# Optimization experiments

Measured on AMD Instinct MI355X. Metric: run time of the kernel, lower is better.

The kernel has to match this reference:

```python
import jax, jax.numpy as jnp
import numpy as np

HIDDEN = 1024
VOCAB = 50257
MAX_LEN = 512


def setup_inputs() -> dict:
    key = jax.random.key(0)
    ks = jax.random.split(key, 16)
    s = 0.02
    return {
        # forward args
        "input_token": jax.random.randint(ks[0], (1,), 0, VOCAB),
        "hidden": jax.random.normal(ks[1], (1, 1, HIDDEN), jnp.float32),
        "encoder_outputs": jax.random.normal(ks[2], (MAX_LEN, HIDDEN), jnp.float32),
        # learned parameters
        "emb": jax.random.normal(ks[3], (VOCAB, HIDDEN), jnp.float32) * s,
        "attn_W": jax.random.normal(ks[4], (MAX_LEN, 2 * HIDDEN), jnp.float32) * s,
        "attn_b": jnp.zeros((MAX_LEN,), jnp.float32),
        "comb_W": jax.random.normal(ks[5], (HIDDEN, 2 * HIDDEN), jnp.float32) * s,
        "comb_b": jnp.zeros((HIDDEN,), jnp.float32),
        "W_ih": jax.random.normal(ks[6], (3 * HIDDEN, HIDDEN), jnp.float32) * s,
        "W_hh": jax.random.normal(ks[7], (3 * HIDDEN, HIDDEN), jnp.float32) * s,
        "b_ih": jnp.zeros((3 * HIDDEN,), jnp.float32),
        "b_hh": jnp.zeros((3 * HIDDEN,), jnp.float32),
        "out_W": jax.random.normal(ks[8], (VOCAB, HIDDEN), jnp.float32) * s,
        "out_b": jnp.zeros((VOCAB,), jnp.float32),
    }


def reference(input_token, hidden, encoder_outputs, emb, attn_W, attn_b,
              comb_W, comb_b, W_ih, W_hh, b_ih, b_hh, out_W, out_b):
    H = hidden.shape[-1]
    # embedding lookup: [1, H]; dropout=0.0 -> identity
    embed = emb[input_token]
    h0 = hidden[0]  # [1, H]
    # Bahdanau-style attention over encoder outputs
    cat = jnp.concatenate([embed, h0], axis=1)                 # [1, 2H]
    attn_weights = jax.nn.softmax(cat @ attn_W.T + attn_b, axis=1)  # [1, L]
    attn_applied = attn_weights @ encoder_outputs              # [1, H]
    # combine + relu
    x = jnp.concatenate([embed, attn_applied], axis=1) @ comb_W.T + comb_b
    x = jax.nn.relu(x)                                         # [1, H]
    # single GRU step (PyTorch gate ordering: r, z, n)
    gi = x @ W_ih.T + b_ih    # [1, 3H]
    gh = h0 @ W_hh.T + b_hh   # [1, 3H]
    i_r, i_z, i_n = gi[:, :H], gi[:, H:2 * H], gi[:, 2 * H:]
    h_r, h_z, h_n = gh[:, :H], gh[:, H:2 * H], gh[:, 2 * H:]
    r = jax.nn.sigmoid(i_r + h_r)
    z = jax.nn.sigmoid(i_z + h_z)
    n = jnp.tanh(i_n + r * h_n)
    h_new = (1.0 - z) * n + z * h0                             # [1, H]
    # output projection + log-softmax
    logp = jax.nn.log_softmax(h_new @ out_W.T + out_b, axis=1)  # [1, V]
    return logp, h_new[None], attn_weights
```

## Files before the change

kernel.cpp:

```cpp
#include <hip/hip_runtime.h>
#include <math.h>

#define H 1024
#define V 50257
#define L 512

#define S_SCORES   0
#define S_ATTN     1024
#define S_X        2048
#define S_GI       3072
#define S_GH       6144
#define S_HNEW     9216
#define S_LOGITS   10240
#define S_PART     60512
#define S_PARTIALS 76928
#define S_RED      102064

#define NB_LOGITS  12565

__device__ __forceinline__ float dot4(float4 a, float4 b) {
  return a.x*b.x + a.y*b.y + a.z*b.z + a.w*b.w;
}

__device__ __forceinline__ float wred_sum(float v) {
  #pragma unroll
  for (int o = 32; o > 0; o >>= 1) v += __shfl_down(v, o, 64);
  return v;
}

__device__ __forceinline__ float wred_max(float v) {
  #pragma unroll
  for (int o = 32; o > 0; o >>= 1) v = fmaxf(v, __shfl_down(v, o, 64));
  return v;
}

__global__ void k_scores(const int* __restrict__ tok, const float* __restrict__ h0,
                         const float* __restrict__ emb, const float* __restrict__ attn_W,
                         const float* __restrict__ attn_b, float* __restrict__ ws) {
  __shared__ float red[4];
  int t = threadIdx.x, lane = t & 63, wid = t >> 6;
  int j = blockIdx.x;
  const float4* wr = (const float4*)(attn_W + (size_t)j * (2 * H));
  const float4* e4 = (const float4*)(emb + (size_t)tok[0] * H);
  const float4* h4 = (const float4*)h0;
  float v = dot4(wr[t], e4[t]) + dot4(wr[256 + t], h4[t]);
  v = wred_sum(v);
  if (lane == 0) red[wid] = v;
  __syncthreads();
  if (t == 0) ws[S_SCORES + j] = red[0] + red[1] + red[2] + red[3] + attn_b[j];
}

__global__ void k_softmax_attn(const float* __restrict__ enc, float* __restrict__ ws,
                               float* __restrict__ out) {
  __shared__ float w[512];
  __shared__ float red[4];
  int t = threadIdx.x, lane = t & 63, wid = t >> 6;
  float s0 = ws[S_SCORES + t], s1 = ws[S_SCORES + 256 + t];
  float m = wred_max(fmaxf(s0, s1));
  if (lane == 0) red[wid] = m;
  __syncthreads();
  m = fmaxf(fmaxf(red[0], red[1]), fmaxf(red[2], red[3]));
  __syncthreads();
  float e0 = expf(s0 - m), e1 = expf(s1 - m);
  float ls = wred_sum(e0 + e1);
  if (lane == 0) red[wid] = ls;
  __syncthreads();
  float inv = 1.0f / (red[0] + red[1] + red[2] + red[3]);
  w[t] = e0 * inv;
  w[256 + t] = e1 * inv;
  __syncthreads();
  if (blockIdx.x == 0) {
    out[V + H + t] = w[t];
    out[V + H + 256 + t] = w[256 + t];
  }
  int cc = blockIdx.x & 3, rc = blockIdx.x >> 2;
  int col = cc * 256 + t;
  int j0 = rc * 32;
  float acc = 0.f;
  #pragma unroll 8
  for (int j = 0; j < 32; ++j) acc += w[j0 + j] * enc[(size_t)(j0 + j) * H + col];
  ws[S_PART + (size_t)rc * H + col] = acc;
}

__global__ void k_attn_reduce(float* __restrict__ ws) {
  int col = blockIdx.x * 256 + threadIdx.x;
  float acc = 0.f;
  #pragma unroll
  for (int p = 0; p < 16; ++p) acc += ws[S_PART + (size_t)p * H + col];
  ws[S_ATTN + col] = acc;
}

__global__ void k_comb(const int* __restrict__ tok, const float* __restrict__ emb,
                       const float* __restrict__ comb_W, const float* __restrict__ comb_b,
                       float* __restrict__ ws) {
  int t = threadIdx.x, lane = t & 63, wid = t >> 6;
  int row = blockIdx.x * 4 + wid;
  const float4* wr = (const float4*)(comb_W + (size_t)row * (2 * H));
  const float4* e4 = (const float4*)(emb + (size_t)tok[0] * H);
  const float4* a4 = (const float4*)(ws + S_ATTN);
  float v = 0.f;
  #pragma unroll
  for (int k = 0; k < 4; ++k) v += dot4(wr[lane + 64 * k], e4[lane + 64 * k]);
  #pragma unroll
  for (int k = 0; k < 4; ++k) v += dot4(wr[256 + lane + 64 * k], a4[lane + 64 * k]);
  v = wred_sum(v);
  if (lane == 0) ws[S_X + row] = fmaxf(v + comb_b[row], 0.f);
}

__global__ void k_gates(const float* __restrict__ h0, const float* __restrict__ W_ih,
                        const float* __restrict__ W_hh, const float* __restrict__ b_ih,
                        const float* __restrict__ b_hh, float* __restrict__ ws) {
  int t = threadIdx.x, lane = t & 63, wid = t >> 6;
  int g = blockIdx.x * 4 + wid;
  const float* Wp;
  const float4* vec;
  float bias;
  int dst;
  if (g < 3 * H) {
    Wp = W_ih + (size_t)g * H;
    vec = (const float4*)(ws + S_X);
    bias = b_ih[g];
    dst = S_GI + g;
  } else {
    int r = g - 3 * H;
    Wp = W_hh + (size_t)r * H;
    vec = (const float4*)h0;
    bias = b_hh[r];
    dst = S_GH + r;
  }
  const float4* wr = (const float4*)Wp;
  float v = 0.f;
  #pragma unroll
  for (int k = 0; k < 4; ++k) v += dot4(wr[lane + 64 * k], vec[lane + 64 * k]);
  v = wred_sum(v);
  if (lane == 0) ws[dst] = v + bias;
}

__global__ void k_gru(const float* __restrict__ h0, float* __restrict__ ws,
                      float* __restrict__ out) {
  int i = blockIdx.x * 256 + threadIdx.x;
  float ir = ws[S_GI + i], iz = ws[S_GI + H + i], in_ = ws[S_GI + 2 * H + i];
  float hr = ws[S_GH + i], hz = ws[S_GH + H + i], hn = ws[S_GH + 2 * H + i];
  float r = 1.f / (1.f + expf(-(ir + hr)));
  float z = 1.f / (1.f + expf(-(iz + hz)));
  float n = tanhf(in_ + r * hn);
  float h = (1.f - z) * n + z * h0[i];
  ws[S_HNEW + i] = h;
  out[V + i] = h;
}

__global__ void k_logits(const float* __restrict__ out_W, const float* __restrict__ out_b,
                         float* __restrict__ ws) {
  __shared__ float hl[H];
  __shared__ float wl[4];
  int t = threadIdx.x, lane = t & 63, wid = t >> 6;
  ((float4*)hl)[t] = ((const float4*)(ws + S_HNEW))[t];
  __syncthreads();
  int row = blockIdx.x * 4 + wid;
  float logit = -INFINITY;
  if (row < V) {
    const float4* wr = (const float4*)(out_W + (size_t)row * H);
    const float4* h4 = (const float4*)hl;
    float v = 0.f;
    #pragma unroll
    for (int k = 0; k < 4; ++k) v += dot4(wr[lane + 64 * k], h4[lane + 64 * k]);
    v = wred_sum(v);
    if (lane == 0) {
      logit = v + out_b[row];
      ws[S_LOGITS + row] = logit;
    }
  }
  if (lane == 0) wl[wid] = logit;
  __syncthreads();
  if (t == 0) {
    float m = fmaxf(fmaxf(wl[0], wl[1]), fmaxf(wl[2], wl[3]));
    float s = 0.f;
    #pragma unroll
    for (int i = 0; i < 4; ++i)
      if (wl[i] != -INFINITY) s += expf(wl[i] - m);
    ws[S_PARTIALS + 2 * blockIdx.x] = m;
    ws[S_PARTIALS + 2 * blockIdx.x + 1] = s;
  }
}

__device__ __forceinline__ void lse_merge(float& m, float& s, float mb, float sb) {
  if (mb == -INFINITY) return;
  if (m == -INFINITY) { m = mb; s = sb; return; }
  if (mb > m) { float tm = m; m = mb; mb = tm; float ts = s; s = sb; sb = ts; }
  s += sb * expf(mb - m);
}

__global__ void k_combine(float* __restrict__ ws) {
  __shared__ float lm[4], lsv[4];
  int t = threadIdx.x, lane = t & 63, wid = t >> 6;
  float m = -INFINITY, s = 0.f;
  for (int i = t; i < NB_LOGITS; i += 256)
    lse_merge(m, s, ws[S_PARTIALS + 2 * i], ws[S_PARTIALS + 2 * i + 1]);
  #pragma unroll
  for (int o = 32; o > 0; o >>= 1) {
    float mb = __shfl_down(m, o, 64);
    float sb = __shfl_down(s, o, 64);
    lse_merge(m, s, mb, sb);
  }
  if (lane == 0) { lm[wid] = m; lsv[wid] = s; }
  __syncthreads();
  if (t == 0) {
    float M = lm[0], S = lsv[0];
    #pragma unroll
    for (int i = 1; i < 4; ++i) lse_merge(M, S, lm[i], lsv[i]);
    ws[S_RED] = M + logf(S);
  }
}

__global__ void k_logp(const float* __restrict__ ws, float* __restrict__ out) {
  int i = blockIdx.x * 256 + threadIdx.x;
  if (i < V) out[i] = ws[S_LOGITS + i] - ws[S_RED];
}

extern "C" void kernel_launch(void* const* d_in, const int* in_sizes, int n_in,
                              void* d_out, int out_size, void* d_ws, size_t ws_size,
                              hipStream_t stream) {
  const int* tok = (const int*)d_in[0];
  const float* hidden = (const float*)d_in[1];
  const float* enc = (const float*)d_in[2];
  const float* emb = (const float*)d_in[3];
  const float* attn_W = (const float*)d_in[4];
  const float* attn_b = (const float*)d_in[5];
  const float* comb_W = (const float*)d_in[6];
  const float* comb_b = (const float*)d_in[7];
  const float* W_ih = (const float*)d_in[8];
  const float* W_hh = (const float*)d_in[9];
  const float* b_ih = (const float*)d_in[10];
  const float* b_hh = (const float*)d_in[11];
  const float* out_W = (const float*)d_in[12];
  const float* out_b = (const float*)d_in[13];
  float* out = (float*)d_out;
  float* ws = (float*)d_ws;

  hipLaunchKernelGGL(k_scores, dim3(512), dim3(256), 0, stream, tok, hidden, emb, attn_W, attn_b, ws);
  hipLaunchKernelGGL(k_softmax_attn, dim3(64), dim3(256), 0, stream, enc, ws, out);
  hipLaunchKernelGGL(k_attn_reduce, dim3(4), dim3(256), 0, stream, ws);
  hipLaunchKernelGGL(k_comb, dim3(256), dim3(256), 0, stream, tok, emb, comb_W, comb_b, ws);
  hipLaunchKernelGGL(k_gates, dim3(1536), dim3(256), 0, stream, hidden, W_ih, W_hh, b_ih, b_hh, ws);
  hipLaunchKernelGGL(k_gru, dim3(4), dim3(256), 0, stream, hidden, ws, out);
  hipLaunchKernelGGL(k_logits, dim3(NB_LOGITS), dim3(256), 0, stream, out_W, out_b, ws);
  hipLaunchKernelGGL(k_combine, dim3(1), dim3(256), 0, stream, ws);
  hipLaunchKernelGGL(k_logp, dim3((V + 255) / 256), dim3(256), 0, stream, ws, out);
}
```

Before: 439.6 us.

## Fuse attention reduce into combine, write logits in place, widen logits blocks

Removes the separate attention-partials reduction kernel by summing the 16 partials inside the combine kernel. Logits are now written straight into the output buffer, and the final kernel subtracts the log-sum-exp in place, which drops a workspace round trip. The logits kernel handles 16 rows per block (4 per wave) to cut block count and partial count, and the scores kernel uses one wave per row. In exchange, the combine kernel repeats the partial reduction in every block, and each wave issues fewer parallel loads, which may lower memory-level parallelism.

```diff
diff --git a/kernel.cpp b/kernel.cpp
--- a/kernel.cpp
+++ b/kernel.cpp
@@ -6,17 +6,15 @@
 #define L 512
 
 #define S_SCORES   0
-#define S_ATTN     1024
 #define S_X        2048
 #define S_GI       3072
 #define S_GH       6144
 #define S_HNEW     9216
-#define S_LOGITS   10240
-#define S_PART     60512
-#define S_PARTIALS 76928
-#define S_RED      102064
-
-#define NB_LOGITS  12565
+#define S_PART     10240
+#define S_PARTIALS 26624
+#define S_RED      33000
+
+#define NB_LOGITS  3142
 
 __device__ __forceinline__ float dot4(float4 a, float4 b) {
   return a.x*b.x + a.y*b.y + a.z*b.z + a.w*b.w;
@@ -37,17 +35,19 @@
 __global__ void k_scores(const int* __restrict__ tok, const float* __restrict__ h0,
                          const float* __restrict__ emb, const float* __restrict__ attn_W,
                          const float* __restrict__ attn_b, float* __restrict__ ws) {
-  __shared__ float red[4];
-  int t = threadIdx.x, lane = t & 63, wid = t >> 6;
-  int j = blockIdx.x;
+  int t = threadIdx.x, lane = t & 63, wid = t >> 6;
+  int j = blockIdx.x * 4 + wid;
   const float4* wr = (const float4*)(attn_W + (size_t)j * (2 * H));
   const float4* e4 = (const float4*)(emb + (size_t)tok[0] * H);
   const float4* h4 = (const float4*)h0;
-  float v = dot4(wr[t], e4[t]) + dot4(wr[256 + t], h4[t]);
+  float v = 0.f;
+  #pragma unroll
+  for (int k = 0; k < 4; ++k) {
+    int idx = lane + 64 * k;
+    v += dot4(wr[idx], e4[idx]) + dot4(wr[256 + idx], h4[idx]);
+  }
   v = wred_sum(v);
-  if (lane == 0) red[wid] = v;
-  __syncthreads();
-  if (t == 0) ws[S_SCORES + j] = red[0] + red[1] + red[2] + red[3] + attn_b[j];
+  if (lane == 0) ws[S_SCORES + j] = v + attn_b[j];
 }
 
 __global__ void k_softmax_attn(const float* __restrict__ enc, float* __restrict__ ws,
@@ -82,14 +82,6 @@
   ws[S_PART + (size_t)rc * H + col] = acc;
 }
 
-__global__ void k_attn_reduce(float* __restrict__ ws) {
-  int col = blockIdx.x * 256 + threadIdx.x;
-  float acc = 0.f;
-  #pragma unroll
-  for (int p = 0; p < 16; ++p) acc += ws[S_PART + (size_t)p * H + col];
-  ws[S_ATTN + col] = acc;
-}
-
 __global__ void k_comb(const int* __restrict__ tok, const float* __restrict__ emb,
                        const float* __restrict__ comb_W, const float* __restrict__ comb_b,
                        float* __restrict__ ws) {
@@ -97,12 +89,20 @@
   int row = blockIdx.x * 4 + wid;
   const float4* wr = (const float4*)(comb_W + (size_t)row * (2 * H));
   const float4* e4 = (const float4*)(emb + (size_t)tok[0] * H);
-  const float4* a4 = (const float4*)(ws + S_ATTN);
+  const float4* p4 = (const float4*)(ws + S_PART);
   float v = 0.f;
   #pragma unroll
-  for (int k = 0; k < 4; ++k) v += dot4(wr[lane + 64 * k], e4[lane + 64 * k]);
-  #pragma unroll
-  for (int k = 0; k < 4; ++k) v += dot4(wr[256 + lane + 64 * k], a4[lane + 64 * k]);
+  for (int k = 0; k < 4; ++k) {
+    int idx = lane + 64 * k;
+    v += dot4(wr[idx], e4[idx]);
+    float4 a = make_float4(0.f, 0.f, 0.f, 0.f);
+    #pragma unroll
+    for (int p = 0; p < 16; ++p) {
+      float4 b = p4[p * 256 + idx];
+      a.x += b.x; a.y += b.y; a.z += b.z; a.w += b.w;
+    }
+    v += dot4(wr[256 + idx], a);
+  }
   v = wred_sum(v);
   if (lane == 0) ws[S_X + row] = fmaxf(v + comb_b[row], 0.f);
 }
@@ -150,33 +150,46 @@
 }
 
 __global__ void k_logits(const float* __restrict__ out_W, const float* __restrict__ out_b,
-                         float* __restrict__ ws) {
+                         float* __restrict__ ws, float* __restrict__ out) {
   __shared__ float hl[H];
-  __shared__ float wl[4];
+  __shared__ float wl[16];
   int t = threadIdx.x, lane = t & 63, wid = t >> 6;
   ((float4*)hl)[t] = ((const float4*)(ws + S_HNEW))[t];
   __syncthreads();
-  int row = blockIdx.x * 4 + wid;
-  float logit = -INFINITY;
-  if (row < V) {
-    const float4* wr = (const float4*)(out_W + (size_t)row * H);
-    const float4* h4 = (const float4*)hl;
+  const float4* h4 = (const float4*)hl;
+  int base = blockIdx.x * 16 + wid * 4;
+  float lg[4];
+  #pragma unroll
+  for (int r = 0; r < 4; ++r) {
+    int row = base + r;
     float v = 0.f;
-    #pragma unroll
-    for (int k = 0; k < 4; ++k) v += dot4(wr[lane + 64 * k], h4[lane + 64 * k]);
+    if (row < V) {
+      const float4* wr = (const float4*)(out_W + (size_t)row * H);
+      #pragma unroll
+      for (int k = 0; k < 4; ++k) {
+        int idx = lane + 64 * k;
+        v += dot4(wr[idx], h4[idx]);
+      }
+    }
     v = wred_sum(v);
-    if (lane == 0) {
-      logit = v + out_b[row];
-      ws[S_LOGITS + row] = logit;
+    lg[r] = -INFINITY;
+    if (lane == 0 && row < V) {
+      lg[r] = v + out_b[row];
+      out[row] = lg[r];
     }
   }
-  if (lane == 0) wl[wid] = logit;
+  if (lane == 0) {
+    #pragma unroll
+    for (int r = 0; r < 4; ++r) wl[wid * 4 + r] = lg[r];
+  }
   __syncthreads();
   if (t == 0) {
-    float m = fmaxf(fmaxf(wl[0], wl[1]), fmaxf(wl[2], wl[3]));
+    float m = -INFINITY;
+    #pragma unroll
+    for (int i = 0; i < 16; ++i) m = fmaxf(m, wl[i]);
     float s = 0.f;
     #pragma unroll
-    for (int i = 0; i < 4; ++i)
+    for (int i = 0; i < 16; ++i)
       if (wl[i] != -INFINITY) s += expf(wl[i] - m);
     ws[S_PARTIALS + 2 * blockIdx.x] = m;
     ws[S_PARTIALS + 2 * blockIdx.x + 1] = s;
@@ -214,7 +227,7 @@
 
 __global__ void k_logp(const float* __restrict__ ws, float* __restrict__ out) {
   int i = blockIdx.x * 256 + threadIdx.x;
-  if (i < V) out[i] = ws[S_LOGITS + i] - ws[S_RED];
+  if (i < V) out[i] -= ws[S_RED];
 }
 
 extern "C" void kernel_launch(void* const* d_in, const int* in_sizes, int n_in,
@@ -237,13 +250,12 @@
   float* out = (float*)d_out;
   float* ws = (float*)d_ws;
 
-  hipLaunchKernelGGL(k_scores, dim3(512), dim3(256), 0, stream, tok, hidden, emb, attn_W, attn_b, ws);
+  hipLaunchKernelGGL(k_scores, dim3(128), dim3(256), 0, stream, tok, hidden, emb, attn_W, attn_b, ws);
   hipLaunchKernelGGL(k_softmax_attn, dim3(64), dim3(256), 0, stream, enc, ws, out);
-  hipLaunchKernelGGL(k_attn_reduce, dim3(4), dim3(256), 0, stream, ws);
   hipLaunchKernelGGL(k_comb, dim3(256), dim3(256), 0, stream, tok, emb, comb_W, comb_b, ws);
   hipLaunchKernelGGL(k_gates, dim3(1536), dim3(256), 0, stream, hidden, W_ih, W_hh, b_ih, b_hh, ws);
   hipLaunchKernelGGL(k_gru, dim3(4), dim3(256), 0, stream, hidden, ws, out);
-  hipLaunchKernelGGL(k_logits, dim3(NB_LOGITS), dim3(256), 0, stream, out_W, out_b, ws);
+  hipLaunchKernelGGL(k_logits, dim3(NB_LOGITS), dim3(256), 0, stream, out_W, out_b, ws, out);
   hipLaunchKernelGGL(k_combine, dim3(1), dim3(256), 0, stream, ws);
   hipLaunchKernelGGL(k_logp, dim3((V + 255) / 256), dim3(256), 0, stream, ws, out);
 }
```

Measured after the change: 430.0 us. -2.2%, faster.
